# Optimization experiments

Measured on AMD Instinct MI355X. Metric: run time of the kernel, lower is better.

## Reference

```python
import jax, jax.numpy as jnp
import numpy as np


def setup_inputs() -> dict:
    key = jax.random.key(0)
    k1, k2, k3 = jax.random.split(key, 3)
    B, S, IN, OUT = 2, 4096, 4096, 11008
    # int8 activations and weights, matching torch.randint(-127, 127, ...)
    x = jax.random.randint(k1, (B, S, IN), -127, 127, dtype=jnp.int8)
    weight = jax.random.randint(k2, (OUT, IN), -127, 127, dtype=jnp.int8)
    bias = jax.random.normal(k3, (1, OUT), dtype=jnp.float32)
    alpha = jnp.array(1e-3, dtype=jnp.float32)  # input_scale * weight_scale
    return {"x": x, "weight": weight, "bias": bias, "alpha": alpha}


def reference(x, weight, bias, alpha):
    # y = SiLU(alpha * (x_i8 @ W_i8^T) + beta * bias), beta = 1.0, output fp32
    x_shape = x.shape
    x2d = x.reshape(-1, x_shape[-1])  # [N, in]
    acc = jnp.matmul(x2d.astype(jnp.int32), weight.T.astype(jnp.int32))  # [N, out] int32
    y = alpha * acc.astype(jnp.float32) + bias  # fused dequant + bias epilogue
    y = y * jax.nn.sigmoid(y)  # SiLU
    return y.reshape(*x_shape[:-1], -1)
```

## Files before the change

kernel.cpp:

```cpp
#include <hip/hip_runtime.h>
#include <stdint.h>

#define TM 128
#define TN 128
#define BK 64

typedef __attribute__((ext_vector_type(4))) int i32x4;

__device__ __forceinline__ void async16(const void* g, void* l) {
    __builtin_amdgcn_global_load_lds(
        (const __attribute__((address_space(1))) unsigned int*)g,
        (__attribute__((address_space(3))) unsigned int*)l,
        16 , 0 , 0 );
}

__global__ void pack_i32_to_i8(const int4* __restrict__ src, int4* __restrict__ dst, int n16) {
    int idx = blockIdx.x * blockDim.x + threadIdx.x;
    int stride = gridDim.x * blockDim.x;
    for (int i = idx; i < n16; i += stride) {
        const int4* s = src + (size_t)i * 4;
        int4 a = s[0], b = s[1], c = s[2], d = s[3];
        int4 o;
        o.x = (a.x & 0xFF) | ((a.y & 0xFF) << 8) | ((a.z & 0xFF) << 16) | (a.w << 24);
        o.y = (b.x & 0xFF) | ((b.y & 0xFF) << 8) | ((b.z & 0xFF) << 16) | (b.w << 24);
        o.z = (c.x & 0xFF) | ((c.y & 0xFF) << 8) | ((c.z & 0xFF) << 16) | (c.w << 24);
        o.w = (d.x & 0xFF) | ((d.y & 0xFF) << 8) | ((d.z & 0xFF) << 16) | (d.w << 24);
        dst[i] = o;
    }
}

__global__ __launch_bounds__(256, 2) void w8a8_silu_kernel(
    const int8_t* __restrict__ x, const int8_t* __restrict__ w,
    const float* __restrict__ bias, const float* __restrict__ alpha_p,
    float* __restrict__ out, int M, int N, int K)
{
    __shared__ int8_t lds_a[TM * BK];
    __shared__ int8_t lds_b[TN * BK];

    const int tid  = threadIdx.x;
    const int lane = tid & 63;
    const int wave = tid >> 6;

    const int srow  = tid >> 2;
    const int skoff = (tid & 3) * 16;

    const size_t bm = blockIdx.y, bn = blockIdx.x;
    const int8_t* ga0 = x + (bm * TM + srow) * (size_t)K + skoff;
    const int8_t* ga1 = ga0 + (size_t)64 * K;
    const int8_t* gb0 = w + (bn * TN + srow) * (size_t)K + skoff;
    const int8_t* gb1 = gb0 + (size_t)64 * K;

    int8_t* la0 = lds_a + tid * 16;
    int8_t* la1 = la0 + 4096;
    int8_t* lb0 = lds_b + tid * 16;
    int8_t* lb1 = lb0 + 4096;

    const int wrow = (wave >> 1) * 64;
    const int wcol = (wave & 1) * 64;
    const int l15  = lane & 15;
    const int quad = lane >> 4;

    i32x4 acc[4][4] = {};

    for (int k0 = 0; k0 < K; k0 += BK) {
        __syncthreads();
        async16(ga0 + k0, la0);
        async16(ga1 + k0, la1);
        async16(gb0 + k0, lb0);
        async16(gb1 + k0, lb1);
        __syncthreads();

        i32x4 af[4], bf[4];
#pragma unroll
        for (int t = 0; t < 4; ++t) {
            af[t] = *(const i32x4*)(lds_a + (wrow + t * 16 + l15) * BK + quad * 16);
            bf[t] = *(const i32x4*)(lds_b + (wcol + t * 16 + l15) * BK + quad * 16);
        }
#pragma unroll
        for (int mt = 0; mt < 4; ++mt)
#pragma unroll
            for (int nt = 0; nt < 4; ++nt)
                acc[mt][nt] = __builtin_amdgcn_mfma_i32_16x16x64_i8(
                    af[mt], bf[nt], acc[mt][nt], 0, 0, 0);
    }

    const float alpha = *alpha_p;
    const int col_base = (int)bn * TN + wcol;
    const int row_base = (int)bm * TM + wrow;

#pragma unroll
    for (int nt = 0; nt < 4; ++nt) {
        const int col = col_base + nt * 16 + l15;
        const float bv = bias[col];
#pragma unroll
        for (int mt = 0; mt < 4; ++mt) {
            const int row0 = row_base + mt * 16 + quad * 4;
#pragma unroll
            for (int r = 0; r < 4; ++r) {
                float y = alpha * (float)acc[mt][nt][r] + bv;
                float s = y / (1.0f + __expf(-y));
                out[(size_t)(row0 + r) * N + col] = s;
            }
        }
    }
}

extern "C" void kernel_launch(void* const* d_in, const int* in_sizes, int n_in,
                              void* d_out, int out_size, void* d_ws, size_t ws_size,
                              hipStream_t stream) {
    const int*   x32   = (const int*)d_in[0];
    const int*   w32   = (const int*)d_in[1];
    const float* bias  = (const float*)d_in[2];
    const float* alpha = (const float*)d_in[3];
    float*       out   = (float*)d_out;

    const int N = in_sizes[2];
    const int K = in_sizes[1] / N;
    const int M = in_sizes[0] / K;

    int8_t* x8 = (int8_t*)d_ws;
    int8_t* w8 = x8 + (size_t)M * K;

    {
        int n16 = (M * (long long)K) / 16;
        pack_i32_to_i8<<<2048, 256, 0, stream>>>((const int4*)x32, (int4*)x8, (int)n16);
    }
    {
        int n16 = ((long long)N * K) / 16;
        pack_i32_to_i8<<<2048, 256, 0, stream>>>((const int4*)w32, (int4*)w8, (int)n16);
    }

    dim3 grid(N / TN, M / TM);
    w8a8_silu_kernel<<<grid, 256, 0, stream>>>(x8, w8, bias, alpha, out, M, N, K);
}
```

Measured before the change: 1.068 ms.

## Switch to 32x32x32 MFMA, BK=128 with XOR-swizzled LDS, XCD remap, fused pack

The K tile doubles to 128, and the 16x16x64 int8 MFMA is replaced by 32x32x32 with a 2x2 accumulator per wave. LDS columns are XOR-swizzled to avoid bank conflicts on the wider rows. Blocks are launched on a 1D grid and remapped so consecutive tiles land on the same XCD, which should improve L2 reuse. The two pack kernels are merged into one launch that converts one int4 per iteration. LDS use doubles to 32KB per block, which may reduce occupancy, and the loop is still single-buffered with syncthreads.

```diff
diff --git a/kernel.cpp b/kernel.cpp
--- a/kernel.cpp
+++ b/kernel.cpp
@@ -3,9 +3,10 @@
 
 #define TM 128
 #define TN 128
-#define BK 64
+#define BK 128
 
-typedef __attribute__((ext_vector_type(4))) int i32x4;
+typedef __attribute__((ext_vector_type(4)))  int i32x4;
+typedef __attribute__((ext_vector_type(16))) int i32x16;
 
 __device__ __forceinline__ void async16(const void* g, void* l) {
     __builtin_amdgcn_global_load_lds(
@@ -14,25 +15,24 @@
         16 , 0 , 0 );
 }
 
-__global__ void pack_i32_to_i8(const int4* __restrict__ src, int4* __restrict__ dst, int n16) {
-    int idx = blockIdx.x * blockDim.x + threadIdx.x;
+__global__ void pack_both(const int4* __restrict__ sx, int* __restrict__ dx, int nx4,
+                          const int4* __restrict__ sw, int* __restrict__ dw, int nw4) {
+    int idx    = blockIdx.x * blockDim.x + threadIdx.x;
     int stride = gridDim.x * blockDim.x;
-    for (int i = idx; i < n16; i += stride) {
-        const int4* s = src + (size_t)i * 4;
-        int4 a = s[0], b = s[1], c = s[2], d = s[3];
-        int4 o;
-        o.x = (a.x & 0xFF) | ((a.y & 0xFF) << 8) | ((a.z & 0xFF) << 16) | (a.w << 24);
-        o.y = (b.x & 0xFF) | ((b.y & 0xFF) << 8) | ((b.z & 0xFF) << 16) | (b.w << 24);
-        o.z = (c.x & 0xFF) | ((c.y & 0xFF) << 8) | ((c.z & 0xFF) << 16) | (c.w << 24);
-        o.w = (d.x & 0xFF) | ((d.y & 0xFF) << 8) | ((d.z & 0xFF) << 16) | (d.w << 24);
-        dst[i] = o;
+    for (int i = idx; i < nx4; i += stride) {
+        int4 a = sx[i];
+        dx[i] = (a.x & 0xFF) | ((a.y & 0xFF) << 8) | ((a.z & 0xFF) << 16) | (a.w << 24);
+    }
+    for (int i = idx; i < nw4; i += stride) {
+        int4 a = sw[i];
+        dw[i] = (a.x & 0xFF) | ((a.y & 0xFF) << 8) | ((a.z & 0xFF) << 16) | (a.w << 24);
     }
 }
 
 __global__ __launch_bounds__(256, 2) void w8a8_silu_kernel(
     const int8_t* __restrict__ x, const int8_t* __restrict__ w,
     const float* __restrict__ bias, const float* __restrict__ alpha_p,
-    float* __restrict__ out, int M, int N, int K)
+    float* __restrict__ out, int M, int N, int K, int nbn)
 {
     __shared__ int8_t lds_a[TM * BK];
     __shared__ int8_t lds_b[TN * BK];
@@ -41,65 +41,66 @@
     const int lane = tid & 63;
     const int wave = tid >> 6;
 
-    const int srow  = tid >> 2;
-    const int skoff = (tid & 3) * 16;
+    int bid = blockIdx.x;
+    const int nwg = gridDim.x;
+    if ((nwg & 7) == 0) bid = (bid & 7) * (nwg >> 3) + (bid >> 3);
+    const int bm = bid / nbn;
+    const int bn = bid - bm * nbn;
 
-    const size_t bm = blockIdx.y, bn = blockIdx.x;
-    const int8_t* ga0 = x + (bm * TM + srow) * (size_t)K + skoff;
-    const int8_t* ga1 = ga0 + (size_t)64 * K;
-    const int8_t* gb0 = w + (bn * TN + srow) * (size_t)K + skoff;
-    const int8_t* gb1 = gb0 + (size_t)64 * K;
+    const int srow  = tid >> 3;
+    const int skoff = (((tid & 7) ^ (srow & 7)) << 4);
+    const int8_t* gA = x + ((size_t)bm * TM + srow) * K + skoff;
+    const int8_t* gB = w + ((size_t)bn * TN + srow) * K + skoff;
+    int8_t* lA = lds_a + tid * 16;
+    int8_t* lB = lds_b + tid * 16;
 
-    int8_t* la0 = lds_a + tid * 16;
-    int8_t* la1 = la0 + 4096;
-    int8_t* lb0 = lds_b + tid * 16;
-    int8_t* lb1 = lb0 + 4096;
+    const int wr  = (wave >> 1) * 64;
+    const int wc  = (wave & 1) * 64;
+    const int l31 = lane & 31;
+    const int q2  = lane >> 5;
+    const int xl  = lane & 7;
 
-    const int wrow = (wave >> 1) * 64;
-    const int wcol = (wave & 1) * 64;
-    const int l15  = lane & 15;
-    const int quad = lane >> 4;
-
-    i32x4 acc[4][4] = {};
+    i32x16 acc[2][2] = {};
 
     for (int k0 = 0; k0 < K; k0 += BK) {
         __syncthreads();
-        async16(ga0 + k0, la0);
-        async16(ga1 + k0, la1);
-        async16(gb0 + k0, lb0);
-        async16(gb1 + k0, lb1);
+#pragma unroll
+        for (int j = 0; j < 4; ++j) {
+            async16(gA + (size_t)(j * 32) * K + k0, lA + j * 4096);
+            async16(gB + (size_t)(j * 32) * K + k0, lB + j * 4096);
+        }
         __syncthreads();
 
-        i32x4 af[4], bf[4];
 #pragma unroll
-        for (int t = 0; t < 4; ++t) {
-            af[t] = *(const i32x4*)(lds_a + (wrow + t * 16 + l15) * BK + quad * 16);
-            bf[t] = *(const i32x4*)(lds_b + (wcol + t * 16 + l15) * BK + quad * 16);
+        for (int ks = 0; ks < 4; ++ks) {
+            i32x4 af[2], bf[2];
+            const int ck = ((ks * 2 + q2) ^ xl) << 4;
+#pragma unroll
+            for (int t = 0; t < 2; ++t) {
+                af[t] = *(const i32x4*)(lds_a + ((wr + t * 32 + l31) << 7) + ck);
+                bf[t] = *(const i32x4*)(lds_b + ((wc + t * 32 + l31) << 7) + ck);
+            }
+            acc[0][0] = __builtin_amdgcn_mfma_i32_32x32x32_i8(af[0], bf[0], acc[0][0], 0, 0, 0);
+            acc[0][1] = __builtin_amdgcn_mfma_i32_32x32x32_i8(af[0], bf[1], acc[0][1], 0, 0, 0);
+            acc[1][0] = __builtin_amdgcn_mfma_i32_32x32x32_i8(af[1], bf[0], acc[1][0], 0, 0, 0);
+            acc[1][1] = __builtin_amdgcn_mfma_i32_32x32x32_i8(af[1], bf[1], acc[1][1], 0, 0, 0);
         }
-#pragma unroll
-        for (int mt = 0; mt < 4; ++mt)
-#pragma unroll
-            for (int nt = 0; nt < 4; ++nt)
-                acc[mt][nt] = __builtin_amdgcn_mfma_i32_16x16x64_i8(
-                    af[mt], bf[nt], acc[mt][nt], 0, 0, 0);
     }
 
     const float alpha = *alpha_p;
-    const int col_base = (int)bn * TN + wcol;
-    const int row_base = (int)bm * TM + wrow;
-
+    const int rowb = bm * TM + wr;
+    const int colb = bn * TN + wc;
 #pragma unroll
-    for (int nt = 0; nt < 4; ++nt) {
-        const int col = col_base + nt * 16 + l15;
+    for (int ct = 0; ct < 2; ++ct) {
+        const int col = colb + ct * 32 + l31;
         const float bv = bias[col];
 #pragma unroll
-        for (int mt = 0; mt < 4; ++mt) {
-            const int row0 = row_base + mt * 16 + quad * 4;
+        for (int rt = 0; rt < 2; ++rt) {
 #pragma unroll
-            for (int r = 0; r < 4; ++r) {
-                float y = alpha * (float)acc[mt][nt][r] + bv;
-                float s = y / (1.0f + __expf(-y));
-                out[(size_t)(row0 + r) * N + col] = s;
+            for (int r = 0; r < 16; ++r) {
+                const int row = rowb + rt * 32 + (r & 3) + ((r >> 2) << 3) + (q2 << 2);
+                float y = fmaf(alpha, (float)acc[rt][ct][r], bv);
+                out[(size_t)row * N + col] = y / (1.0f + __expf(-y));
             }
         }
     }
@@ -121,15 +122,11 @@
     int8_t* x8 = (int8_t*)d_ws;
     int8_t* w8 = x8 + (size_t)M * K;
 
-    {
-        int n16 = (M * (long long)K) / 16;
-        pack_i32_to_i8<<<2048, 256, 0, stream>>>((const int4*)x32, (int4*)x8, (int)n16);
-    }
-    {
-        int n16 = ((long long)N * K) / 16;
-        pack_i32_to_i8<<<2048, 256, 0, stream>>>((const int4*)w32, (int4*)w8, (int)n16);
-    }
+    const int nx4 = (int)(((size_t)M * K) / 4);
+    const int nw4 = (int)(((size_t)N * K) / 4);
+    pack_both<<<2048, 256, 0, stream>>>((const int4*)x32, (int*)x8, nx4,
+                                        (const int4*)w32, (int*)w8, nw4);
 
-    dim3 grid(N / TN, M / TM);
-    w8a8_silu_kernel<<<grid, 256, 0, stream>>>(x8, w8, bias, alpha, out, M, N, K);
+    const int nbm = M / TM, nbn = N / TN;
+    w8a8_silu_kernel<<<nbm * nbn, 256, 0, stream>>>(x8, w8, bias, alpha, out, M, N, K, nbn);
 }
```

Result: faster. 982.7 us (-7.9%).
